# Performance work log

Measured on AMD Instinct MI355X. Metric: run time of the kernel, lower is better.

Reference implementation:

```python
import jax, jax.numpy as jnp
import numpy as np

NEG_SLOPE = 0.2  # DGL GATConv default leaky_relu slope


def gat_conv(x, src, dst, W, attn_l, attn_r, bias, res_W):
    """DGL GATConv (eval mode, residual=True with linear res_fc, bias).
    x: [N, F_in]; src/dst: [E]; W: [F_in, H*D]; attn_l/r: [H, D];
    bias: [H*D]; res_W: [F_in, H*D]. Returns [N, H, D]."""
    N = x.shape[0]
    H, D = attn_l.shape
    feat = (x @ W).reshape(N, H, D)
    el = jnp.sum(feat * attn_l, axis=-1)  # [N, H]
    er = jnp.sum(feat * attn_r, axis=-1)  # [N, H]
    e = jax.nn.leaky_relu(el[src] + er[dst], NEG_SLOPE)  # [E, H]
    # edge softmax over incoming edges of each dst node (numerically stable)
    m = jnp.full((N, H), -jnp.inf, dtype=e.dtype).at[dst].max(e)
    ex = jnp.exp(e - m[dst])
    s = jnp.zeros((N, H), dtype=e.dtype).at[dst].add(ex)
    alpha = ex / s[dst]  # [E, H]
    # scatter-aggregate messages alpha * feat[src] into dst
    rst = jnp.zeros((N, H, D), dtype=x.dtype).at[dst].add(alpha[:, :, None] * feat[src])
    rst = rst + (x @ res_W).reshape(N, H, D) + bias.reshape(1, H, D)
    return rst


def setup_inputs() -> dict:
    key = jax.random.key(0)
    N, E, F_IN, HID, OUT, H = 20000, 320000, 128, 128, 128, 4
    ks = jax.random.split(key, 32)
    ki = iter(range(32))

    def rn(shape, scale=0.05):
        return jax.random.normal(ks[next(ki)], shape, dtype=jnp.float32) * scale

    inp = {
        "n_feat": jax.random.normal(ks[next(ki)], (N, F_IN), dtype=jnp.float32),
        "src": jax.random.randint(ks[next(ki)], (E,), 0, N, dtype=jnp.int32),
        "dst": jax.random.randint(ks[next(ki)], (E,), 0, N, dtype=jnp.int32),
        # input GATConv: F_IN -> H x HID
        "W0": rn((F_IN, H * HID)), "al0": rn((H, HID)), "ar0": rn((H, HID)),
        "b0": rn((H * HID,)), "rW0": rn((F_IN, H * HID)),
        "DW0": rn((H * HID, HID)), "Db0": rn((HID,)),
        # middle GATConv: HID -> H x HID
        "W1": rn((HID, H * HID)), "al1": rn((H, HID)), "ar1": rn((H, HID)),
        "b1": rn((H * HID,)), "rW1": rn((HID, H * HID)),
        "DW1": rn((H * HID, HID)), "Db1": rn((HID,)),
        # output GATConv: HID -> H x OUT
        "W2": rn((HID, H * OUT)), "al2": rn((H, OUT)), "ar2": rn((H, OUT)),
        "b2": rn((H * OUT,)), "rW2": rn((HID, H * OUT)),
    }
    return inp


def reference(n_feat, src, dst,
              W0, al0, ar0, b0, rW0, DW0, Db0,
              W1, al1, ar1, b1, rW1, DW1, Db1,
              W2, al2, ar2, b2, rW2):
    N = n_feat.shape[0]
    relu = jax.nn.relu
    # input GAT block
    h = relu(gat_conv(n_feat, src, dst, W0, al0, ar0, b0, rW0))  # [N, H, HID]
    h = relu(h.reshape(N, -1) @ DW0 + Db0)                        # [N, HID]
    # middle GAT block
    h = relu(gat_conv(h, src, dst, W1, al1, ar1, b1, rW1))
    h = relu(h.reshape(N, -1) @ DW1 + Db1)
    # output GAT + head-mean + graph max pooling (single graph)
    h = relu(gat_conv(h, src, dst, W2, al2, ar2, b2, rW2))        # [N, H, OUT]
    h = relu(jnp.mean(h, axis=-2))                                 # [N, OUT]
    return jnp.max(h, axis=0, keepdims=True)                       # [1, OUT]
```

## Files before the change

### kernel.cpp

```cpp
#include <hip/hip_runtime.h>
#include <hip/hip_bf16.h>


typedef __attribute__((ext_vector_type(8))) short bf16x8;
typedef __attribute__((ext_vector_type(4))) float f32x4;
typedef __hip_bfloat16 bf16_t;

__global__ __launch_bounds__(256) void prep_weights(
    const float* __restrict__ W0, const float* __restrict__ rW0,
    const float* __restrict__ W1, const float* __restrict__ rW1,
    const float* __restrict__ W2, const float* __restrict__ rW2,
    const float* __restrict__ DW0, const float* __restrict__ DW1,
    bf16_t* __restrict__ out) {
  int idx = blockIdx.x * 256 + threadIdx.x;
  float v;
  if (idx < 393216) {
    int mat = idx / 131072;
    int off = idx & 131071;
    int n = off >> 7, k = off & 127;
    const float* W = (mat == 0) ? W0 : (mat == 1) ? W1 : W2;
    const float* rW = (mat == 0) ? rW0 : (mat == 1) ? rW1 : rW2;
    v = (n < 512) ? W[k * 512 + n] : rW[k * 512 + (n - 512)];
  } else {
    int rem = idx - 393216;
    int mat = rem >> 16;
    int off = rem & 65535;
    int n = off >> 9, k = off & 511;
    const float* DW = mat ? DW1 : DW0;
    v = DW[k * 128 + n];
  }
  out[idx] = __float2bfloat16(v);
}

__global__ __launch_bounds__(256) void convert_bf16(const float* __restrict__ in,
                                                    bf16_t* __restrict__ out, int n) {
  int i = (blockIdx.x * 256 + threadIdx.x) * 4;
  if (i < n) {
    float4 v = *(const float4*)(in + i);
    out[i + 0] = __float2bfloat16(v.x);
    out[i + 1] = __float2bfloat16(v.y);
    out[i + 2] = __float2bfloat16(v.z);
    out[i + 3] = __float2bfloat16(v.w);
  }
}

__global__ __launch_bounds__(256) void mfma_gemm128(
    const bf16_t* __restrict__ A, const bf16_t* __restrict__ Bt,
    bf16_t* __restrict__ C, int M, int ldc, int K) {
  __shared__ bf16_t As[128 * 40];
  __shared__ bf16_t Bs[128 * 40];
  int tid = threadIdx.x;
  int lane = tid & 63, wave = tid >> 6;
  int q = lane >> 4, r16 = lane & 15;
  int wm = (wave >> 1) * 64, wn = (wave & 1) * 64;
  int rowBase = blockIdx.y * 128, colBase = blockIdx.x * 128;

  f32x4 acc[4][4] = {};

  for (int k0 = 0; k0 < K; k0 += 32) {
#pragma unroll
    for (int t = 0; t < 2; t++) {
      int s = tid + t * 256;
      int row = s >> 2, kq = (s & 3) * 8;
      int gr = rowBase + row;
      bf16x8 va = {};
      if (gr < M) va = *(const bf16x8*)(A + (size_t)gr * K + k0 + kq);
      *(bf16x8*)(As + row * 40 + kq) = va;
      bf16x8 vb = *(const bf16x8*)(Bt + (size_t)(colBase + row) * K + k0 + kq);
      *(bf16x8*)(Bs + row * 40 + kq) = vb;
    }
    __syncthreads();
    bf16x8 af[4], bfr[4];
#pragma unroll
    for (int i = 0; i < 4; i++)
      af[i] = *(const bf16x8*)(As + (wm + i * 16 + r16) * 40 + q * 8);
#pragma unroll
    for (int j = 0; j < 4; j++)
      bfr[j] = *(const bf16x8*)(Bs + (wn + j * 16 + r16) * 40 + q * 8);
#pragma unroll
    for (int i = 0; i < 4; i++)
#pragma unroll
      for (int j = 0; j < 4; j++)
        acc[i][j] = __builtin_amdgcn_mfma_f32_16x16x32_bf16(af[i], bfr[j], acc[i][j], 0, 0, 0);
    __syncthreads();
  }

#pragma unroll
  for (int j = 0; j < 4; j++) {
    int col = colBase + wn + j * 16 + r16;
#pragma unroll
    for (int i = 0; i < 4; i++) {
#pragma unroll
      for (int r = 0; r < 4; r++) {
        int row = rowBase + wm + i * 16 + q * 4 + r;
        if (row < M) C[(size_t)row * ldc + col] = __float2bfloat16(acc[i][j][r]);
      }
    }
  }
}

__global__ __launch_bounds__(256) void mfma_gemm64(
    const bf16_t* __restrict__ A, const bf16_t* __restrict__ Bt,
    const float* __restrict__ bias, bf16_t* __restrict__ C,
    int M, int ldc, int K) {
  __shared__ bf16_t As[64 * 40];
  __shared__ bf16_t Bs[64 * 40];
  int tid = threadIdx.x;
  int lane = tid & 63, wave = tid >> 6;
  int q = lane >> 4, r16 = lane & 15;
  int wm = (wave >> 1) * 32, wn = (wave & 1) * 32;
  int rowBase = blockIdx.y * 64, colBase = blockIdx.x * 64;
  int row = tid >> 2, kq = (tid & 3) * 8;

  f32x4 acc[2][2] = {};

  for (int k0 = 0; k0 < K; k0 += 32) {
    int gr = rowBase + row;
    bf16x8 va = {};
    if (gr < M) va = *(const bf16x8*)(A + (size_t)gr * K + k0 + kq);
    *(bf16x8*)(As + row * 40 + kq) = va;
    bf16x8 vb = *(const bf16x8*)(Bt + (size_t)(colBase + row) * K + k0 + kq);
    *(bf16x8*)(Bs + row * 40 + kq) = vb;
    __syncthreads();
    bf16x8 af[2], bfr[2];
#pragma unroll
    for (int i = 0; i < 2; i++)
      af[i] = *(const bf16x8*)(As + (wm + i * 16 + r16) * 40 + q * 8);
#pragma unroll
    for (int j = 0; j < 2; j++)
      bfr[j] = *(const bf16x8*)(Bs + (wn + j * 16 + r16) * 40 + q * 8);
#pragma unroll
    for (int i = 0; i < 2; i++)
#pragma unroll
      for (int j = 0; j < 2; j++)
        acc[i][j] = __builtin_amdgcn_mfma_f32_16x16x32_bf16(af[i], bfr[j], acc[i][j], 0, 0, 0);
    __syncthreads();
  }

#pragma unroll
  for (int j = 0; j < 2; j++) {
    int col = colBase + wn + j * 16 + r16;
    float bb = bias[col];
#pragma unroll
    for (int i = 0; i < 2; i++) {
#pragma unroll
      for (int r = 0; r < 4; r++) {
        int rw = rowBase + wm + i * 16 + q * 4 + r;
        if (rw < M) C[(size_t)rw * ldc + col] = __float2bfloat16(fmaxf(acc[i][j][r] + bb, 0.f));
      }
    }
  }
}

__global__ __launch_bounds__(256) void el_er_kernel(
    const bf16_t* __restrict__ fused, const float* __restrict__ al,
    const float* __restrict__ ar, float* __restrict__ el,
    float* __restrict__ er, int N) {
  int n = blockIdx.x;
  int h = threadIdx.x >> 6;
  int l = threadIdx.x & 63;
  unsigned int fp = *(const unsigned int*)(fused + (size_t)n * 1024 + h * 128 + l * 2);
  float f0 = __uint_as_float(fp << 16);
  float f1 = __uint_as_float(fp & 0xffff0000u);
  const float2 av = *(const float2*)(al + h * 128 + l * 2);
  const float2 bv = *(const float2*)(ar + h * 128 + l * 2);
  float sl = f0 * av.x + f1 * av.y;
  float sr = f0 * bv.x + f1 * bv.y;
  for (int off = 32; off; off >>= 1) {
    sl += __shfl_down(sl, off);
    sr += __shfl_down(sr, off);
  }
  if (l == 0) {
    el[n * 4 + h] = sl;
    er[n * 4 + h] = sr;
  }
}

__global__ __launch_bounds__(256) void count_kernel(const int* __restrict__ dst,
                                                    int* __restrict__ counts, int E) {
  int i = blockIdx.x * blockDim.x + threadIdx.x;
  if (i < E) atomicAdd(&counts[dst[i]], 1);
}

__global__ __launch_bounds__(1024) void scan_kernel(const int* __restrict__ counts,
                                                    int* __restrict__ row_ptr,
                                                    int* __restrict__ cursor, int N) {
  __shared__ int sums[1024];
  int t = threadIdx.x;
  int chunk = (N + 1023) / 1024;
  int begin = t * chunk;
  int end = begin + chunk;
  if (end > N) end = N;
  int s = 0;
  for (int i = begin; i < end; i++) s += counts[i];
  sums[t] = s;
  __syncthreads();
  for (int off = 1; off < 1024; off <<= 1) {
    int v = (t >= off) ? sums[t - off] : 0;
    __syncthreads();
    sums[t] += v;
    __syncthreads();
  }
  int run = (t == 0) ? 0 : sums[t - 1];
  for (int i = begin; i < end; i++) {
    row_ptr[i] = run;
    cursor[i] = run;
    run += counts[i];
  }
  if (t == 1023) row_ptr[N] = sums[1023];
}

__global__ __launch_bounds__(256) void scatter_kernel(
    const int* __restrict__ src, const int* __restrict__ dst,
    int* __restrict__ cursor, int* __restrict__ edge_src, int E) {
  int i = blockIdx.x * blockDim.x + threadIdx.x;
  if (i < E) {
    int d = dst[i];
    int pos = atomicAdd(&cursor[d], 1);
    edge_src[pos] = src[i];
  }
}

__global__ __launch_bounds__(256) void gat_agg_kernel(
    const bf16_t* __restrict__ fused,
    const float* __restrict__ el, const float* __restrict__ er,
    const float* __restrict__ bias, const int* __restrict__ row_ptr,
    const int* __restrict__ edge_src, bf16_t* __restrict__ out, int N) {
  int n = blockIdx.x;
  int h = threadIdx.x >> 6;
  int l = threadIdx.x & 63;
  int g = l >> 4, t = l & 15;
  int start = row_ptr[n];
  int deg = row_ptr[n + 1] - start;
  float er_nh = er[n * 4 + h];

  float m = -3.402823466e38f;
  for (int i = l; i < deg; i += 64) {
    int s = edge_src[start + i];
    float e = el[s * 4 + h] + er_nh;
    e = (e > 0.f) ? e : 0.2f * e;
    m = fmaxf(m, e);
  }
#pragma unroll
  for (int off = 32; off; off >>= 1) m = fmaxf(m, __shfl_xor(m, off));

  float acc[8] = {};
  float ssum = 0.f;
  for (int i = g; i < deg; i += 4) {
    int s = edge_src[start + i];
    float e = el[s * 4 + h] + er_nh;
    e = (e > 0.f) ? e : 0.2f * e;
    float w = __expf(e - m);
    ssum += w;
    uint4 fp = *(const uint4*)(fused + (size_t)s * 1024 + h * 128 + t * 8);
    unsigned int u0 = fp.x, u1 = fp.y, u2 = fp.z, u3 = fp.w;
    acc[0] += w * __uint_as_float(u0 << 16);
    acc[1] += w * __uint_as_float(u0 & 0xffff0000u);
    acc[2] += w * __uint_as_float(u1 << 16);
    acc[3] += w * __uint_as_float(u1 & 0xffff0000u);
    acc[4] += w * __uint_as_float(u2 << 16);
    acc[5] += w * __uint_as_float(u2 & 0xffff0000u);
    acc[6] += w * __uint_as_float(u3 << 16);
    acc[7] += w * __uint_as_float(u3 & 0xffff0000u);
  }
#pragma unroll
  for (int off = 16; off <= 32; off <<= 1) {
    ssum += __shfl_xor(ssum, off);
#pragma unroll
    for (int d = 0; d < 8; d++) acc[d] += __shfl_xor(acc[d], off);
  }

  if (g == 0) {
    float inv = (deg > 0) ? 1.f / ssum : 0.f;
    uint4 rp = *(const uint4*)(fused + (size_t)n * 1024 + 512 + h * 128 + t * 8);
    const float* bp = bias + h * 128 + t * 8;
    unsigned int ru[4] = {rp.x, rp.y, rp.z, rp.w};
    unsigned int ow[4];
#pragma unroll
    for (int j = 0; j < 4; j++) {
      float o0 = fmaxf(acc[2 * j] * inv + __uint_as_float(ru[j] << 16) + bp[2 * j], 0.f);
      float o1 = fmaxf(acc[2 * j + 1] * inv + __uint_as_float(ru[j] & 0xffff0000u) + bp[2 * j + 1], 0.f);
      ow[j] = (((unsigned int)__bfloat16_as_ushort(__float2bfloat16(o1))) << 16) |
              (unsigned int)__bfloat16_as_ushort(__float2bfloat16(o0));
    }
    *(uint4*)(out + (size_t)n * 512 + h * 128 + t * 8) = make_uint4(ow[0], ow[1], ow[2], ow[3]);
  }
}

__global__ __launch_bounds__(128) void pool_kernel(const bf16_t* __restrict__ g,
                                                   float* __restrict__ out, int N) {
  int d = threadIdx.x;
  float mx = 0.f;
  for (int n = blockIdx.x; n < N; n += gridDim.x) {
    const bf16_t* p = g + (size_t)n * 512 + d;
    float v = 0.25f * (__bfloat162float(p[0]) + __bfloat162float(p[128]) +
                       __bfloat162float(p[256]) + __bfloat162float(p[384]));
    mx = fmaxf(mx, v);
  }
  atomicMax((int*)out + d, __float_as_int(mx));
}

extern "C" void kernel_launch(void* const* d_in, const int* in_sizes, int n_in,
                              void* d_out, int out_size, void* d_ws, size_t ws_size,
                              hipStream_t stream) {
  const float* n_feat = (const float*)d_in[0];
  const int* src = (const int*)d_in[1];
  const int* dst = (const int*)d_in[2];
  const float* W0 = (const float*)d_in[3];
  const float* al0 = (const float*)d_in[4];
  const float* ar0 = (const float*)d_in[5];
  const float* b0 = (const float*)d_in[6];
  const float* rW0 = (const float*)d_in[7];
  const float* DW0 = (const float*)d_in[8];
  const float* Db0 = (const float*)d_in[9];
  const float* W1 = (const float*)d_in[10];
  const float* al1 = (const float*)d_in[11];
  const float* ar1 = (const float*)d_in[12];
  const float* b1 = (const float*)d_in[13];
  const float* rW1 = (const float*)d_in[14];
  const float* DW1 = (const float*)d_in[15];
  const float* Db1 = (const float*)d_in[16];
  const float* W2 = (const float*)d_in[17];
  const float* al2 = (const float*)d_in[18];
  const float* ar2 = (const float*)d_in[19];
  const float* b2 = (const float*)d_in[20];
  const float* rW2 = (const float*)d_in[21];

  const int N = in_sizes[0] / 128;
  const int E = in_sizes[1];

  bf16_t* xbf = (bf16_t*)d_ws;
  bf16_t* fusedFR = xbf + (size_t)N * 128;
  bf16_t* outC = fusedFR + (size_t)N * 1024;
  bf16_t* denseD = outC + (size_t)N * 512;
  bf16_t* wts = denseD + (size_t)N * 128;
  float* el = (float*)(wts + 524288);
  float* er = el + (size_t)N * 4;
  int* counts = (int*)(er + (size_t)N * 4);
  int* row_ptr = counts + N;
  int* cursor = row_ptr + (N + 1);
  int* edge_src = cursor + N;

  bf16_t* FW0 = wts;
  bf16_t* FW1 = wts + 131072;
  bf16_t* FW2 = wts + 262144;
  bf16_t* DWt0 = wts + 393216;
  bf16_t* DWt1 = wts + 458752;

  prep_weights<<<2048, 256, 0, stream>>>(W0, rW0, W1, rW1, W2, rW2, DW0, DW1, wts);
  convert_bf16<<<(N * 128 / 4 + 255) / 256, 256, 0, stream>>>(n_feat, xbf, N * 128);

  hipMemsetAsync(counts, 0, (size_t)N * sizeof(int), stream);
  count_kernel<<<(E + 255) / 256, 256, 0, stream>>>(dst, counts, E);
  scan_kernel<<<1, 1024, 0, stream>>>(counts, row_ptr, cursor, N);
  scatter_kernel<<<(E + 255) / 256, 256, 0, stream>>>(src, dst, cursor, edge_src, E);

  dim3 gF(8, (N + 127) / 128);
  dim3 gD(2, (N + 63) / 64);

  mfma_gemm128<<<gF, 256, 0, stream>>>(xbf, FW0, fusedFR, N, 1024, 128);
  el_er_kernel<<<N, 256, 0, stream>>>(fusedFR, al0, ar0, el, er, N);
  gat_agg_kernel<<<N, 256, 0, stream>>>(fusedFR, el, er, b0, row_ptr, edge_src, outC, N);
  mfma_gemm64<<<gD, 256, 0, stream>>>(outC, DWt0, Db0, denseD, N, 128, 512);

  mfma_gemm128<<<gF, 256, 0, stream>>>(denseD, FW1, fusedFR, N, 1024, 128);
  el_er_kernel<<<N, 256, 0, stream>>>(fusedFR, al1, ar1, el, er, N);
  gat_agg_kernel<<<N, 256, 0, stream>>>(fusedFR, el, er, b1, row_ptr, edge_src, outC, N);
  mfma_gemm64<<<gD, 256, 0, stream>>>(outC, DWt1, Db1, denseD, N, 128, 512);

  mfma_gemm128<<<gF, 256, 0, stream>>>(denseD, FW2, fusedFR, N, 1024, 128);
  el_er_kernel<<<N, 256, 0, stream>>>(fusedFR, al2, ar2, el, er, N);
  gat_agg_kernel<<<N, 256, 0, stream>>>(fusedFR, el, er, b2, row_ptr, edge_src, outC, N);

  hipMemsetAsync(d_out, 0, 128 * sizeof(float), stream);
  pool_kernel<<<256, 128, 0, stream>>>(outC, (float*)d_out, N);
}
```

Baseline: 514.3 us.

## Precompute W·attn vectors for el/er, widen GEMM K-tile, pack bf16 stores

```diff
diff --git a/kernel.cpp b/kernel.cpp
--- a/kernel.cpp
+++ b/kernel.cpp
@@ -5,6 +5,11 @@
 typedef __attribute__((ext_vector_type(8))) short bf16x8;
 typedef __attribute__((ext_vector_type(4))) float f32x4;
 typedef __hip_bfloat16 bf16_t;
+
+__device__ __forceinline__ unsigned int pack_bf16(float lo, float hi) {
+  return (((unsigned int)__bfloat16_as_ushort(__float2bfloat16(hi))) << 16) |
+         (unsigned int)__bfloat16_as_ushort(__float2bfloat16(lo));
+}
 
 __global__ __launch_bounds__(256) void prep_weights(
     const float* __restrict__ W0, const float* __restrict__ rW0,
@@ -32,6 +37,26 @@
   out[idx] = __float2bfloat16(v);
 }
 
+__global__ __launch_bounds__(256) void alr_kernel(
+    const float* __restrict__ W0, const float* __restrict__ W1,
+    const float* __restrict__ W2, const float* __restrict__ al0,
+    const float* __restrict__ ar0, const float* __restrict__ al1,
+    const float* __restrict__ ar1, const float* __restrict__ al2,
+    const float* __restrict__ ar2, float* __restrict__ ALR) {
+  int idx = blockIdx.x * 256 + threadIdx.x;
+  if (idx >= 3 * 128 * 8) return;
+  int L = idx >> 10;
+  int k = (idx >> 3) & 127;
+  int c = idx & 7;
+  int h = c & 3;
+  const float* W = (L == 0) ? W0 : (L == 1) ? W1 : W2;
+  const float* a = (c < 4) ? ((L == 0) ? al0 : (L == 1) ? al1 : al2)
+                           : ((L == 0) ? ar0 : (L == 1) ? ar1 : ar2);
+  float s = 0.f;
+  for (int d = 0; d < 128; d++) s += W[k * 512 + h * 128 + d] * a[h * 128 + d];
+  ALR[idx] = s;
+}
+
 __global__ __launch_bounds__(256) void convert_bf16(const float* __restrict__ in,
                                                     bf16_t* __restrict__ out, int n) {
   int i = (blockIdx.x * 256 + threadIdx.x) * 4;
@@ -47,8 +72,8 @@
 __global__ __launch_bounds__(256) void mfma_gemm128(
     const bf16_t* __restrict__ A, const bf16_t* __restrict__ Bt,
     bf16_t* __restrict__ C, int M, int ldc, int K) {
-  __shared__ bf16_t As[128 * 40];
-  __shared__ bf16_t Bs[128 * 40];
+  __shared__ bf16_t As[128 * 72];
+  __shared__ bf16_t Bs[128 * 72];
   int tid = threadIdx.x;
   int lane = tid & 63, wave = tid >> 6;
   int q = lane >> 4, r16 = lane & 15;
@@ -57,43 +82,55 @@
 
   f32x4 acc[4][4] = {};
 
-  for (int k0 = 0; k0 < K; k0 += 32) {
-#pragma unroll
-    for (int t = 0; t < 2; t++) {
-      int s = tid + t * 256;
-      int row = s >> 2, kq = (s & 3) * 8;
+  for (int k0 = 0; k0 < K; k0 += 64) {
+#pragma unroll
+    for (int p = 0; p < 4; p++) {
+      int s = tid + p * 256;
+      int row = s >> 3, kq = (s & 7) * 8;
       int gr = rowBase + row;
       bf16x8 va = {};
       if (gr < M) va = *(const bf16x8*)(A + (size_t)gr * K + k0 + kq);
-      *(bf16x8*)(As + row * 40 + kq) = va;
+      *(bf16x8*)(As + row * 72 + kq) = va;
       bf16x8 vb = *(const bf16x8*)(Bt + (size_t)(colBase + row) * K + k0 + kq);
-      *(bf16x8*)(Bs + row * 40 + kq) = vb;
-    }
-    __syncthreads();
-    bf16x8 af[4], bfr[4];
-#pragma unroll
-    for (int i = 0; i < 4; i++)
-      af[i] = *(const bf16x8*)(As + (wm + i * 16 + r16) * 40 + q * 8);
-#pragma unroll
-    for (int j = 0; j < 4; j++)
-      bfr[j] = *(const bf16x8*)(Bs + (wn + j * 16 + r16) * 40 + q * 8);
-#pragma unroll
-    for (int i = 0; i < 4; i++)
+      *(bf16x8*)(Bs + row * 72 + kq) = vb;
+    }
+    __syncthreads();
+#pragma unroll
+    for (int ks = 0; ks < 64; ks += 32) {
+      bf16x8 af[4], bfr[4];
+#pragma unroll
+      for (int i = 0; i < 4; i++)
+        af[i] = *(const bf16x8*)(As + (wm + i * 16 + r16) * 72 + ks + q * 8);
 #pragma unroll
       for (int j = 0; j < 4; j++)
-        acc[i][j] = __builtin_amdgcn_mfma_f32_16x16x32_bf16(af[i], bfr[j], acc[i][j], 0, 0, 0);
-    __syncthreads();
-  }
-
-#pragma unroll
-  for (int j = 0; j < 4; j++) {
-    int col = colBase + wn + j * 16 + r16;
-#pragma unroll
-    for (int i = 0; i < 4; i++) {
-#pragma unroll
-      for (int r = 0; r < 4; r++) {
-        int row = rowBase + wm + i * 16 + q * 4 + r;
-        if (row < M) C[(size_t)row * ldc + col] = __float2bfloat16(acc[i][j][r]);
+        bfr[j] = *(const bf16x8*)(Bs + (wn + j * 16 + r16) * 72 + ks + q * 8);
+#pragma unroll
+      for (int i = 0; i < 4; i++)
+#pragma unroll
+        for (int j = 0; j < 4; j++)
+          acc[i][j] = __builtin_amdgcn_mfma_f32_16x16x32_bf16(af[i], bfr[j], acc[i][j], 0, 0, 0);
+    }
+    __syncthreads();
+  }
+
+  int odd = lane & 1;
+  int colb0 = r16 & ~1;
+#pragma unroll
+  for (int i = 0; i < 4; i++) {
+#pragma unroll
+    for (int r = 0; r < 4; r++) {
+      int row = rowBase + wm + i * 16 + q * 4 + r;
+#pragma unroll
+      for (int jp = 0; jp < 2; jp++) {
+        float a0 = acc[i][2 * jp][r];
+        float a1 = acc[i][2 * jp + 1][r];
+        float p0 = __shfl_xor(a0, 1);
+        float p1 = __shfl_xor(a1, 1);
+        float lo = odd ? p1 : a0;
+        float hi = odd ? a1 : p0;
+        int col = colBase + wn + (2 * jp + odd) * 16 + colb0;
+        if (row < M)
+          *(unsigned int*)(C + (size_t)row * ldc + col) = pack_bf16(lo, hi);
       }
     }
   }
@@ -103,76 +140,93 @@
     const bf16_t* __restrict__ A, const bf16_t* __restrict__ Bt,
     const float* __restrict__ bias, bf16_t* __restrict__ C,
     int M, int ldc, int K) {
-  __shared__ bf16_t As[64 * 40];
-  __shared__ bf16_t Bs[64 * 40];
+  __shared__ bf16_t As[64 * 72];
+  __shared__ bf16_t Bs[64 * 72];
   int tid = threadIdx.x;
   int lane = tid & 63, wave = tid >> 6;
   int q = lane >> 4, r16 = lane & 15;
   int wm = (wave >> 1) * 32, wn = (wave & 1) * 32;
   int rowBase = blockIdx.y * 64, colBase = blockIdx.x * 64;
-  int row = tid >> 2, kq = (tid & 3) * 8;
 
   f32x4 acc[2][2] = {};
 
-  for (int k0 = 0; k0 < K; k0 += 32) {
-    int gr = rowBase + row;
-    bf16x8 va = {};
-    if (gr < M) va = *(const bf16x8*)(A + (size_t)gr * K + k0 + kq);
-    *(bf16x8*)(As + row * 40 + kq) = va;
-    bf16x8 vb = *(const bf16x8*)(Bt + (size_t)(colBase + row) * K + k0 + kq);
-    *(bf16x8*)(Bs + row * 40 + kq) = vb;
-    __syncthreads();
-    bf16x8 af[2], bfr[2];
-#pragma unroll
-    for (int i = 0; i < 2; i++)
-      af[i] = *(const bf16x8*)(As + (wm + i * 16 + r16) * 40 + q * 8);
-#pragma unroll
-    for (int j = 0; j < 2; j++)
-      bfr[j] = *(const bf16x8*)(Bs + (wn + j * 16 + r16) * 40 + q * 8);
-#pragma unroll
-    for (int i = 0; i < 2; i++)
+  for (int k0 = 0; k0 < K; k0 += 64) {
+#pragma unroll
+    for (int p = 0; p < 2; p++) {
+      int s = tid + p * 256;
+      int row = s >> 3, kq = (s & 7) * 8;
+      int gr = rowBase + row;
+      bf16x8 va = {};
+      if (gr < M) va = *(const bf16x8*)(A + (size_t)gr * K + k0 + kq);
+      *(bf16x8*)(As + row * 72 + kq) = va;
+      bf16x8 vb = *(const bf16x8*)(Bt + (size_t)(colBase + row) * K + k0 + kq);
+      *(bf16x8*)(Bs + row * 72 + kq) = vb;
+    }
+    __syncthreads();
+#pragma unroll
+    for (int ks = 0; ks < 64; ks += 32) {
+      bf16x8 af[2], bfr[2];
+#pragma unroll
+      for (int i = 0; i < 2; i++)
+        af[i] = *(const bf16x8*)(As + (wm + i * 16 + r16) * 72 + ks + q * 8);
 #pragma unroll
       for (int j = 0; j < 2; j++)
-        acc[i][j] = __builtin_amdgcn_mfma_f32_16x16x32_bf16(af[i], bfr[j], acc[i][j], 0, 0, 0);
-    __syncthreads();
-  }
-
-#pragma unroll
-  for (int j = 0; j < 2; j++) {
-    int col = colBase + wn + j * 16 + r16;
-    float bb = bias[col];
-#pragma unroll
-    for (int i = 0; i < 2; i++) {
-#pragma unroll
-      for (int r = 0; r < 4; r++) {
-        int rw = rowBase + wm + i * 16 + q * 4 + r;
-        if (rw < M) C[(size_t)rw * ldc + col] = __float2bfloat16(fmaxf(acc[i][j][r] + bb, 0.f));
+        bfr[j] = *(const bf16x8*)(Bs + (wn + j * 16 + r16) * 72 + ks + q * 8);
+#pragma unroll
+      for (int i = 0; i < 2; i++)
+#pragma unroll
+        for (int j = 0; j < 2; j++)
+          acc[i][j] = __builtin_amdgcn_mfma_f32_16x16x32_bf16(af[i], bfr[j], acc[i][j], 0, 0, 0);
+    }
+    __syncthreads();
+  }
+
+  int odd = lane & 1;
+  int colb0 = r16 & ~1;
+#pragma unroll
+  for (int i = 0; i < 2; i++) {
+#pragma unroll
+    for (int r = 0; r < 4; r++) {
+      int row = rowBase + wm + i * 16 + q * 4 + r;
+      float a0 = acc[i][0][r];
+      float a1 = acc[i][1][r];
+      float p0 = __shfl_xor(a0, 1);
+      float p1 = __shfl_xor(a1, 1);
+      float lo = odd ? p1 : a0;
+      float hi = odd ? a1 : p0;
+      int col = colBase + wn + odd * 16 + colb0;
+      if (row < M) {
+        float o0 = fmaxf(lo + bias[col], 0.f);
+        float o1 = fmaxf(hi + bias[col + 1], 0.f);
+        *(unsigned int*)(C + (size_t)row * ldc + col) = pack_bf16(o0, o1);
       }
     }
   }
 }
 
-__global__ __launch_bounds__(256) void el_er_kernel(
-    const bf16_t* __restrict__ fused, const float* __restrict__ al,
-    const float* __restrict__ ar, float* __restrict__ el,
-    float* __restrict__ er, int N) {
-  int n = blockIdx.x;
-  int h = threadIdx.x >> 6;
-  int l = threadIdx.x & 63;
-  unsigned int fp = *(const unsigned int*)(fused + (size_t)n * 1024 + h * 128 + l * 2);
-  float f0 = __uint_as_float(fp << 16);
-  float f1 = __uint_as_float(fp & 0xffff0000u);
-  const float2 av = *(const float2*)(al + h * 128 + l * 2);
-  const float2 bv = *(const float2*)(ar + h * 128 + l * 2);
-  float sl = f0 * av.x + f1 * av.y;
-  float sr = f0 * bv.x + f1 * bv.y;
-  for (int off = 32; off; off >>= 1) {
-    sl += __shfl_down(sl, off);
-    sr += __shfl_down(sr, off);
-  }
+__global__ __launch_bounds__(256) void el_er_fast(
+    const bf16_t* __restrict__ x, const float* __restrict__ ALR,
+    float* __restrict__ el, float* __restrict__ er, int N) {
+  int wave = threadIdx.x >> 6, l = threadIdx.x & 63;
+  int n = blockIdx.x * 4 + wave;
+  if (n >= N) return;
+  unsigned int xp = *(const unsigned int*)(x + (size_t)n * 128 + 2 * l);
+  float f0 = __uint_as_float(xp << 16);
+  float f1 = __uint_as_float(xp & 0xffff0000u);
+  const float* A0 = ALR + (size_t)(2 * l) * 8;
+  float s[8];
+#pragma unroll
+  for (int c = 0; c < 8; c++) s[c] = f0 * A0[c] + f1 * A0[8 + c];
+#pragma unroll
+  for (int off = 32; off; off >>= 1)
+#pragma unroll
+    for (int c = 0; c < 8; c++) s[c] += __shfl_xor(s[c], off);
   if (l == 0) {
-    el[n * 4 + h] = sl;
-    er[n * 4 + h] = sr;
+#pragma unroll
+    for (int h = 0; h < 4; h++) {
+      el[n * 4 + h] = s[h];
+      er[n * 4 + h] = s[4 + h];
+    }
   }
 }
 
@@ -280,8 +334,7 @@
     for (int j = 0; j < 4; j++) {
       float o0 = fmaxf(acc[2 * j] * inv + __uint_as_float(ru[j] << 16) + bp[2 * j], 0.f);
       float o1 = fmaxf(acc[2 * j + 1] * inv + __uint_as_float(ru[j] & 0xffff0000u) + bp[2 * j + 1], 0.f);
-      ow[j] = (((unsigned int)__bfloat16_as_ushort(__float2bfloat16(o1))) << 16) |
-              (unsigned int)__bfloat16_as_ushort(__float2bfloat16(o0));
+      ow[j] = pack_bf16(o0, o1);
     }
     *(uint4*)(out + (size_t)n * 512 + h * 128 + t * 8) = make_uint4(ow[0], ow[1], ow[2], ow[3]);
   }
@@ -334,7 +387,8 @@
   bf16_t* outC = fusedFR + (size_t)N * 1024;
   bf16_t* denseD = outC + (size_t)N * 512;
   bf16_t* wts = denseD + (size_t)N * 128;
-  float* el = (float*)(wts + 524288);
+  float* ALR = (float*)(wts + 524288);
+  float* el = ALR + 3072;
   float* er = el + (size_t)N * 4;
   int* counts = (int*)(er + (size_t)N * 4);
   int* row_ptr = counts + N;
@@ -348,6 +402,7 @@
   bf16_t* DWt1 = wts + 458752;
 
   prep_weights<<<2048, 256, 0, stream>>>(W0, rW0, W1, rW1, W2, rW2, DW0, DW1, wts);
+  alr_kernel<<<12, 256, 0, stream>>>(W0, W1, W2, al0, ar0, al1, ar1, al2, ar2, ALR);
   convert_bf16<<<(N * 128 / 4 + 255) / 256, 256, 0, stream>>>(n_feat, xbf, N * 128);
 
   hipMemsetAsync(counts, 0, (size_t)N * sizeof(int), stream);
@@ -357,19 +412,20 @@
 
   dim3 gF(8, (N + 127) / 128);
   dim3 gD(2, (N + 63) / 64);
+  int gEL = (N + 3) / 4;
 
   mfma_gemm128<<<gF, 256, 0, stream>>>(xbf, FW0, fusedFR, N, 1024, 128);
-  el_er_kernel<<<N, 256, 0, stream>>>(fusedFR, al0, ar0, el, er, N);
+  el_er_fast<<<gEL, 256, 0, stream>>>(xbf, ALR, el, er, N);
   gat_agg_kernel<<<N, 256, 0, stream>>>(fusedFR, el, er, b0, row_ptr, edge_src, outC, N);
   mfma_gemm64<<<gD, 256, 0, stream>>>(outC, DWt0, Db0, denseD, N, 128, 512);
 
   mfma_gemm128<<<gF, 256, 0, stream>>>(denseD, FW1, fusedFR, N, 1024, 128);
-  el_er_kernel<<<N, 256, 0, stream>>>(fusedFR, al1, ar1, el, er, N);
+  el_er_fast<<<gEL, 256, 0, stream>>>(denseD, ALR + 1024, el, er, N);
   gat_agg_kernel<<<N, 256, 0, stream>>>(fusedFR, el, er, b1, row_ptr, edge_src, outC, N);
   mfma_gemm64<<<gD, 256, 0, stream>>>(outC, DWt1, Db1, denseD, N, 128, 512);
 
   mfma_gemm128<<<gF, 256, 0, stream>>>(denseD, FW2, fusedFR, N, 1024, 128);
-  el_er_kernel<<<N, 256, 0, stream>>>(fusedFR, al2, ar2, el, er, N);
+  el_er_fast<<<gEL, 256, 0, stream>>>(denseD, ALR + 2048, el, er, N);
   gat_agg_kernel<<<N, 256, 0, stream>>>(fusedFR, el, er, b2, row_ptr, edge_src, outC, N);
 
   hipMemsetAsync(d_out, 0, 128 * sizeof(float), stream);
```

New measurement: 521.4 us. Within noise of the previous version (+1.4%).
